# Performance work log

Measured on AMD Instinct MI355X. Metric: run time of the kernel, lower is better.

## Reference

```python
import jax, jax.numpy as jnp
import numpy as np

D_MODEL = 1024
NUM_HEADS = 16
D_LATENT = 256
HEAD_DIM = D_MODEL // NUM_HEADS
BATCH = 2048
SEQ = 32


def setup_inputs() -> dict:
    key = jax.random.key(0)
    ks = jax.random.split(key, 9)
    s = 1.0 / np.sqrt(D_MODEL)
    sl = 1.0 / np.sqrt(D_LATENT)
    return {
        "x": jax.random.normal(ks[0], (BATCH, SEQ, D_MODEL), dtype=jnp.float32),
        "memory": jax.random.normal(ks[1], (BATCH, SEQ, D_LATENT), dtype=jnp.float32),
        "W_q": jax.random.normal(ks[2], (D_MODEL, D_MODEL), dtype=jnp.float32) * s,
        "W_k": jax.random.normal(ks[3], (D_MODEL, D_MODEL), dtype=jnp.float32) * s,
        "W_v": jax.random.normal(ks[4], (D_MODEL, D_MODEL), dtype=jnp.float32) * s,
        "W_o": jax.random.normal(ks[5], (D_MODEL, D_MODEL), dtype=jnp.float32) * s,
        "W_down_kv": jax.random.normal(ks[6], (D_MODEL, D_LATENT), dtype=jnp.float32) * s,
        "W_up_k": jax.random.normal(ks[7], (D_LATENT, D_MODEL), dtype=jnp.float32) * sl,
        "W_up_v": jax.random.normal(ks[8], (D_LATENT, D_MODEL), dtype=jnp.float32) * sl,
    }


def reference(x, memory, W_q, W_k, W_v, W_o, W_down_kv, W_up_k, W_up_v):
    B, S, _ = x.shape
    q = x @ W_q                     # [B,S,D]
    k = x @ W_k
    v = x @ W_v
    latent_kv = (k + v) @ W_down_kv  # [B,S,L]
    latent_kv = jnp.nan_to_num((latent_kv + memory) * 0.5)
    k_rec = latent_kv @ W_up_k       # [B,S,D]
    v_rec = latent_kv @ W_up_v
    # split heads: [B,H,S,hd]
    qh = q.reshape(B, S, NUM_HEADS, HEAD_DIM).transpose(0, 2, 1, 3)
    kh = k_rec.reshape(B, S, NUM_HEADS, HEAD_DIM).transpose(0, 2, 1, 3)
    vh = v_rec.reshape(B, S, NUM_HEADS, HEAD_DIM).transpose(0, 2, 1, 3)
    # NOTE: faithful to source — scale is sqrt(d_model), not sqrt(head_dim)
    scores = jnp.einsum("bhqd,bhkd->bhqk", qh, kh) / jnp.sqrt(jnp.float32(D_MODEL))
    scores = jnp.nan_to_num(scores, nan=0.0, posinf=10.0, neginf=-10.0)
    attn = jax.nn.softmax(scores, axis=-1)
    ctx = jnp.einsum("bhqk,bhkd->bhqd", attn, vh)
    ctx = ctx.transpose(0, 2, 1, 3).reshape(B, S, D_MODEL)
    out = ctx @ W_o
    return out, latent_kv
```

## Files before the change

### kernel.cpp

```cpp
#include <hip/hip_runtime.h>
#include <hip/hip_bf16.h>

typedef unsigned short u16;
typedef unsigned int u32;
typedef __attribute__((ext_vector_type(8))) __bf16 bf16x8;
typedef __attribute__((ext_vector_type(8))) unsigned short u16x8;
typedef __attribute__((ext_vector_type(4))) float floatx4;
typedef __attribute__((ext_vector_type(16))) float floatx16;

#define AS1 __attribute__((address_space(1)))
#define AS3 __attribute__((address_space(3)))

__device__ __forceinline__ u16 f2bf(float f) {
  unsigned u = __float_as_uint(f);
  u += 0x7fffu + ((u >> 16) & 1u);
  return (u16)(u >> 16);
}

__device__ __forceinline__ void g2lds16(const u16* g, u16* l) {
  __builtin_amdgcn_global_load_lds((AS1 void*)g, (AS3 void*)l, 16, 0, 0);
}

__device__ __forceinline__ void tcvt_body(const float* __restrict__ s,
                                          u16* __restrict__ d, int R, int C,
                                          int bx, int by, int tid,
                                          float (*t)[33]) {
  const int lx = tid & 31, ly = tid >> 5;
  const int x0 = bx * 32, y0 = by * 32;
  #pragma unroll
  for (int i = 0; i < 32; i += 8)
    t[ly + i][lx] = s[(size_t)(y0 + ly + i) * C + x0 + lx];
  __syncthreads();
  #pragma unroll
  for (int i = 0; i < 32; i += 8)
    d[(size_t)(x0 + ly + i) * R + y0 + lx] = f2bf(t[lx][ly + i]);
}

__global__ __launch_bounds__(256) void k_prep(
    const float* __restrict__ x, u16* __restrict__ Xb,
    const float* __restrict__ Wk, const float* __restrict__ Wv, u16* __restrict__ Wkv,
    const float* __restrict__ Wq, u16* __restrict__ WAt,
    const float* __restrict__ Wdn, u16* __restrict__ Wdt,
    const float* __restrict__ Wuk, u16* __restrict__ WBt,
    const float* __restrict__ Wuv, u16* __restrict__ WBt2,
    const float* __restrict__ Wo, u16* __restrict__ Wot) {
  __shared__ float t[32][33];
  const int b = blockIdx.x;
  const int tid = threadIdx.x;
  if (b < 4096) {
    long i = ((long)b * 256 + tid) * 8;
    const long stride = (long)4096 * 256 * 8;
    for (; i < 67108864L; i += stride) {
      float4 a = *(const float4*)(x + i);
      float4 c = *(const float4*)(x + i + 4);
      u16x8 o;
      o[0] = f2bf(a.x); o[1] = f2bf(a.y); o[2] = f2bf(a.z); o[3] = f2bf(a.w);
      o[4] = f2bf(c.x); o[5] = f2bf(c.y); o[6] = f2bf(c.z); o[7] = f2bf(c.w);
      *(u16x8*)(Xb + i) = o;
    }
  } else if (b < 4608) {
    long i = ((long)(b - 4096) * 256 + tid) * 8;
    float4 a0 = *(const float4*)(Wk + i);
    float4 a1 = *(const float4*)(Wk + i + 4);
    float4 b0 = *(const float4*)(Wv + i);
    float4 b1 = *(const float4*)(Wv + i + 4);
    u16x8 o;
    o[0] = f2bf(a0.x + b0.x); o[1] = f2bf(a0.y + b0.y);
    o[2] = f2bf(a0.z + b0.z); o[3] = f2bf(a0.w + b0.w);
    o[4] = f2bf(a1.x + b1.x); o[5] = f2bf(a1.y + b1.y);
    o[6] = f2bf(a1.z + b1.z); o[7] = f2bf(a1.w + b1.w);
    *(u16x8*)(Wkv + i) = o;
  } else if (b < 5632) {
    int lb = b - 4608;
    tcvt_body(Wq, WAt, 1024, 1024, lb & 31, lb >> 5, tid, t);
  } else if (b < 5888) {
    int lb = b - 5632;
    tcvt_body(Wdn, Wdt, 1024, 256, lb & 7, lb >> 3, tid, t);
  } else if (b < 6144) {
    int lb = b - 5888;
    tcvt_body(Wuk, WBt, 256, 1024, lb & 31, lb >> 5, tid, t);
  } else if (b < 6400) {
    int lb = b - 6144;
    tcvt_body(Wuv, WBt2, 256, 1024, lb & 31, lb >> 5, tid, t);
  } else {
    int lb = b - 6400;
    tcvt_body(Wo, Wot, 1024, 1024, lb & 31, lb >> 5, tid, t);
  }
}

#define MFMA16(a, b, c) c = __builtin_amdgcn_mfma_f32_16x16x32_bf16(a, b, c, 0, 0, 0)

template <int MODE>
__global__ __launch_bounds__(512, 4) void gemm_mn(
    const u16* __restrict__ A, const u16* __restrict__ Bt,
    int M, int N, int K, int ntn,
    u16* __restrict__ Cb, float* __restrict__ Cf,
    const float* __restrict__ memp, float* __restrict__ latf, u16* __restrict__ latb) {
  __shared__ u16 As[256 * 64];
  __shared__ u16 Bs[128 * 64];
  const int tid = threadIdx.x;
  const int lane = tid & 63;
  const int wid = tid >> 6;
  const int wr = wid >> 1, wc = wid & 1;

  int bid = blockIdx.x;
  {
    const int nwg = gridDim.x;
    const int q = nwg >> 3, r = nwg & 7;
    const int xcd = bid & 7, idx = bid >> 3;
    bid = (xcd < r ? xcd * (q + 1) : r * (q + 1) + (xcd - r) * q) + idx;
  }
  const int mt = bid / ntn, nt = bid % ntn;
  const int m0 = mt * 256, n0 = nt * 128;

  const int fr = lane & 15;
  const int g8 = (lane >> 4) * 8;
  const int xr = (lane & 7) * 8;

  floatx4 acc[4][4];
  #pragma unroll
  for (int i = 0; i < 4; i++)
    #pragma unroll
    for (int j = 0; j < 4; j++) acc[i][j] = 0.0f;

  const u16* Ag0 = A + (size_t)m0 * K;
  const u16* Bg0 = Bt + (size_t)n0 * K;

  for (int kt = 0; kt < K; kt += 64) {
    #pragma unroll
    for (int p = 0; p < 4; p++) {
      int ci = p * 512 + tid;
      int row = ci >> 3;
      int kc = ((ci & 7) ^ (row & 7)) * 8;
      g2lds16(Ag0 + (size_t)row * K + kt + kc, &As[ci * 8]);
    }
    #pragma unroll
    for (int p = 0; p < 2; p++) {
      int ci = p * 512 + tid;
      int row = ci >> 3;
      int kc = ((ci & 7) ^ (row & 7)) * 8;
      g2lds16(Bg0 + (size_t)row * K + kt + kc, &Bs[ci * 8]);
    }
    __syncthreads();
    #pragma unroll
    for (int kk = 0; kk < 64; kk += 32) {
      const int koff = kk + g8;
      bf16x8 af[4], bfv[4];
      #pragma unroll
      for (int i = 0; i < 4; i++)
        af[i] = *(const bf16x8*)&As[(wr * 64 + i * 16 + fr) * 64 + (koff ^ xr)];
      #pragma unroll
      for (int j = 0; j < 4; j++)
        bfv[j] = *(const bf16x8*)&Bs[(wc * 64 + j * 16 + fr) * 64 + (koff ^ xr)];
      #pragma unroll
      for (int i = 0; i < 4; i++)
        #pragma unroll
        for (int j = 0; j < 4; j++)
          MFMA16(af[i], bfv[j], acc[i][j]);
    }
    __syncthreads();
  }

  #pragma unroll
  for (int i = 0; i < 4; i++) {
    const int mb = m0 + wr * 64 + i * 16 + ((lane >> 4) * 4);
    #pragma unroll
    for (int j = 0; j < 4; j++) {
      const int cb = n0 + wc * 64 + j * 16 + (lane & 15);
      #pragma unroll
      for (int r = 0; r < 4; r++) {
        const int m = mb + r;
        const float v = acc[i][j][r];
        if (MODE == 0) {
          Cb[(size_t)m * N + cb] = f2bf(v);
        } else if (MODE == 1) {
          if (n0 < 1024) {
            Cb[(size_t)m * 1024 + cb] = f2bf(v);
          } else {
            int lc = cb - 1024;
            float lv = (v + memp[(size_t)m * 256 + lc]) * 0.5f;
            latf[(size_t)m * 256 + lc] = lv;
            latb[(size_t)m * 256 + lc] = f2bf(lv);
          }
        } else {
          Cf[(size_t)m * N + cb] = v;
        }
      }
    }
  }
}

__global__ __launch_bounds__(256) void k_attn(const u16* __restrict__ KV, u16* Q) {
  __shared__ u16 Qs[4][32][72];
  __shared__ u16 Ks[4][32][72];
  __shared__ u16 Vt[4][64][40];
  const int tid = threadIdx.x;
  const int hg = blockIdx.x;
  const int b = blockIdx.y;
  const long tok0 = (long)b * 32;

  {
    const int t = tid >> 3, ci = tid & 7;
    const int hd = ci >> 1, c0 = (ci & 1) * 32;
    const u16* qrow = Q + (tok0 + t) * 1024 + hg * 256 + ci * 32;
    #pragma unroll
    for (int u = 0; u < 4; u++)
      *(u16x8*)&Qs[hd][t][c0 + u * 8] = *(const u16x8*)(qrow + u * 8);
    const u16* krow = KV + (tok0 + t) * 2048 + hg * 256 + ci * 32;
    #pragma unroll
    for (int u = 0; u < 4; u++)
      *(u16x8*)&Ks[hd][t][c0 + u * 8] = *(const u16x8*)(krow + u * 8);
    const u16* vrow = KV + (tok0 + t) * 2048 + 1024 + hg * 256 + ci * 32;
    #pragma unroll
    for (int u = 0; u < 4; u++) {
      u16x8 v = *(const u16x8*)(vrow + u * 8);
      #pragma unroll
      for (int j = 0; j < 8; j++) Vt[hd][c0 + u * 8 + j][t] = v[j];
    }
  }
  __syncthreads();

  const int w = tid >> 6;
  const int lane = tid & 63;
  const int col = lane & 31, hi = lane >> 5;

  floatx16 S;
  #pragma unroll
  for (int r = 0; r < 16; r++) S[r] = 0.0f;
  #pragma unroll
  for (int kc = 0; kc < 4; kc++) {
    bf16x8 aq = *(const bf16x8*)&Qs[w][col][kc * 16 + hi * 8];
    bf16x8 bk = *(const bf16x8*)&Ks[w][col][kc * 16 + hi * 8];
    S = __builtin_amdgcn_mfma_f32_32x32x16_bf16(aq, bk, S, 0, 0, 0);
  }

  u16* Pw = &Qs[w][0][0];
  float pr[16];
  #pragma unroll
  for (int r = 0; r < 16; r++) {
    float sc = S[r] * 0.03125f;
    float mx = sc;
    #pragma unroll
    for (int off = 16; off >= 1; off >>= 1) mx = fmaxf(mx, __shfl_xor(mx, off, 64));
    float e = __expf(sc - mx);
    float sm = e;
    #pragma unroll
    for (int off = 16; off >= 1; off >>= 1) sm += __shfl_xor(sm, off, 64);
    pr[r] = e / sm;
  }
  #pragma unroll
  for (int r = 0; r < 16; r++) {
    int row = (r & 3) + 8 * (r >> 2) + 4 * hi;
    Pw[row * 40 + col] = f2bf(pr[r]);
  }
  __syncthreads();

  floatx16 c0v, c1v;
  #pragma unroll
  for (int r = 0; r < 16; r++) { c0v[r] = 0.0f; c1v[r] = 0.0f; }
  #pragma unroll
  for (int kc = 0; kc < 2; kc++) {
    bf16x8 ap = *(const bf16x8*)&Pw[col * 40 + kc * 16 + hi * 8];
    bf16x8 bv0 = *(const bf16x8*)&Vt[w][col][kc * 16 + hi * 8];
    bf16x8 bv1 = *(const bf16x8*)&Vt[w][32 + col][kc * 16 + hi * 8];
    c0v = __builtin_amdgcn_mfma_f32_32x32x16_bf16(ap, bv0, c0v, 0, 0, 0);
    c1v = __builtin_amdgcn_mfma_f32_32x32x16_bf16(ap, bv1, c1v, 0, 0, 0);
  }
  #pragma unroll
  for (int r = 0; r < 16; r++) {
    int row = (r & 3) + 8 * (r >> 2) + 4 * hi;
    u16* orow = Q + (tok0 + row) * 1024 + hg * 256 + w * 64;
    orow[col] = f2bf(c0v[r]);
    orow[col + 32] = f2bf(c1v[r]);
  }
}

extern "C" void kernel_launch(void* const* d_in, const int* in_sizes, int n_in,
                              void* d_out, int out_size, void* d_ws, size_t ws_size,
                              hipStream_t stream) {
  const float* x    = (const float*)d_in[0];
  const float* mem  = (const float*)d_in[1];
  const float* W_q  = (const float*)d_in[2];
  const float* W_k  = (const float*)d_in[3];
  const float* W_v  = (const float*)d_in[4];
  const float* W_o  = (const float*)d_in[5];
  const float* W_dn = (const float*)d_in[6];
  const float* W_uk = (const float*)d_in[7];
  const float* W_uv = (const float*)d_in[8];
  float* out  = (float*)d_out;
  float* latf = out + (size_t)67108864;

  char* wp = (char*)d_ws;
  u16* Qb  = (u16*)wp; wp += (size_t)65536 * 1024 * 2;
  u16* Lb  = (u16*)wp; wp += (size_t)65536 * 256 * 2;
  u16* WAt = (u16*)wp; wp += (size_t)1280 * 1024 * 2;
  u16* WBt = (u16*)wp; wp += (size_t)2048 * 256 * 2;
  u16* Wot = (u16*)wp; wp += (size_t)1024 * 1024 * 2;
  u16* Wdt = (u16*)wp; wp += (size_t)256 * 1024 * 2;
  u16* Wkv = (u16*)wp; wp += (size_t)1024 * 1024 * 2;

  u16* Xb  = (u16*)d_out;
  u16* KVb = (u16*)d_out;

  dim3 b256(256);
  dim3 b512(512);

  k_prep<<<7424, b256, 0, stream>>>(
      x, Xb, W_k, W_v, Wkv, W_q, WAt, W_dn, Wdt,
      W_uk, WBt, W_uv, WBt + (size_t)1024 * 256, W_o, Wot);

  gemm_mn<0><<<8, b512, 0, stream>>>(
      Wdt, Wkv, 256, 1024, 1024, 8, WAt + (size_t)1024 * 1024,
      nullptr, nullptr, nullptr, nullptr);

  gemm_mn<1><<<2560, b512, 0, stream>>>(
      Xb, WAt, 65536, 1280, 1024, 10, Qb, nullptr, mem, latf, Lb);

  gemm_mn<0><<<4096, b512, 0, stream>>>(
      Lb, WBt, 65536, 2048, 256, 16, KVb, nullptr, nullptr, nullptr, nullptr);

  k_attn<<<dim3(4, 2048), b256, 0, stream>>>(KVb, Qb);

  gemm_mn<2><<<2048, b512, 0, stream>>>(
      Qb, Wot, 65536, 1024, 1024, 8, nullptr, out, nullptr, nullptr, nullptr);
}
```

Before: 841.3 us.

## Fuse latent up-projection into attention kernel and shrink GEMM tiles to 128x128

Removes the separate up-projection GEMM that wrote K and V (65536x2048 bf16) to global memory. The attention kernel now loads the latent rows into LDS and computes per-head K and V with MFMA, reading the weights directly from global memory. Separately, the generic GEMM moves from 256x128 tiles with 512 threads to 128x128 tiles with 256 threads, doubling the grid. The fused version recomputes K/V per head group from uncached global weight loads and uses more LDS. It also drops the barrier before the P*V step, which is safe only because each wave reads just its own LDS region.

```diff
diff --git a/kernel.cpp b/kernel.cpp
--- a/kernel.cpp
+++ b/kernel.cpp
@@ -89,14 +89,15 @@
 }
 
 #define MFMA16(a, b, c) c = __builtin_amdgcn_mfma_f32_16x16x32_bf16(a, b, c, 0, 0, 0)
+#define MFMA32(a, b, c) c = __builtin_amdgcn_mfma_f32_32x32x16_bf16(a, b, c, 0, 0, 0)
 
 template <int MODE>
-__global__ __launch_bounds__(512, 4) void gemm_mn(
+__global__ __launch_bounds__(256, 3) void gemm128(
     const u16* __restrict__ A, const u16* __restrict__ Bt,
     int M, int N, int K, int ntn,
     u16* __restrict__ Cb, float* __restrict__ Cf,
     const float* __restrict__ memp, float* __restrict__ latf, u16* __restrict__ latb) {
-  __shared__ u16 As[256 * 64];
+  __shared__ u16 As[128 * 64];
   __shared__ u16 Bs[128 * 64];
   const int tid = threadIdx.x;
   const int lane = tid & 63;
@@ -111,7 +112,7 @@
     bid = (xcd < r ? xcd * (q + 1) : r * (q + 1) + (xcd - r) * q) + idx;
   }
   const int mt = bid / ntn, nt = bid % ntn;
-  const int m0 = mt * 256, n0 = nt * 128;
+  const int m0 = mt * 128, n0 = nt * 128;
 
   const int fr = lane & 15;
   const int g8 = (lane >> 4) * 8;
@@ -129,14 +130,14 @@
   for (int kt = 0; kt < K; kt += 64) {
     #pragma unroll
     for (int p = 0; p < 4; p++) {
-      int ci = p * 512 + tid;
+      int ci = p * 256 + tid;
       int row = ci >> 3;
       int kc = ((ci & 7) ^ (row & 7)) * 8;
       g2lds16(Ag0 + (size_t)row * K + kt + kc, &As[ci * 8]);
     }
     #pragma unroll
-    for (int p = 0; p < 2; p++) {
-      int ci = p * 512 + tid;
+    for (int p = 0; p < 4; p++) {
+      int ci = p * 256 + tid;
       int row = ci >> 3;
       int kc = ((ci & 7) ^ (row & 7)) * 8;
       g2lds16(Bg0 + (size_t)row * K + kt + kc, &Bs[ci * 8]);
@@ -190,10 +191,15 @@
   }
 }
 
-__global__ __launch_bounds__(256) void k_attn(const u16* __restrict__ KV, u16* Q) {
+__global__ __launch_bounds__(256, 2) void k_attn_kv(
+    const u16* __restrict__ Lb,
+    u16* __restrict__ Q,
+    const u16* __restrict__ WBt)
+{
   __shared__ u16 Qs[4][32][72];
   __shared__ u16 Ks[4][32][72];
   __shared__ u16 Vt[4][64][40];
+  __shared__ u16 Ls[32][264];
   const int tid = threadIdx.x;
   const int hg = blockIdx.x;
   const int b = blockIdx.y;
@@ -206,23 +212,47 @@
     #pragma unroll
     for (int u = 0; u < 4; u++)
       *(u16x8*)&Qs[hd][t][c0 + u * 8] = *(const u16x8*)(qrow + u * 8);
-    const u16* krow = KV + (tok0 + t) * 2048 + hg * 256 + ci * 32;
+    const u16* lrow = Lb + (tok0 + t) * 256 + ci * 32;
     #pragma unroll
     for (int u = 0; u < 4; u++)
-      *(u16x8*)&Ks[hd][t][c0 + u * 8] = *(const u16x8*)(krow + u * 8);
-    const u16* vrow = KV + (tok0 + t) * 2048 + 1024 + hg * 256 + ci * 32;
-    #pragma unroll
-    for (int u = 0; u < 4; u++) {
-      u16x8 v = *(const u16x8*)(vrow + u * 8);
-      #pragma unroll
-      for (int j = 0; j < 8; j++) Vt[hd][c0 + u * 8 + j][t] = v[j];
-    }
+      *(u16x8*)&Ls[t][ci * 32 + u * 8] = *(const u16x8*)(lrow + u * 8);
   }
   __syncthreads();
 
   const int w = tid >> 6;
   const int lane = tid & 63;
   const int col = lane & 31, hi = lane >> 5;
+  const int h = hg * 4 + w;
+
+  floatx16 ka0, ka1, va0, va1;
+  #pragma unroll
+  for (int r = 0; r < 16; r++) { ka0[r] = 0.f; ka1[r] = 0.f; va0[r] = 0.f; va1[r] = 0.f; }
+  const u16* wkp = WBt + (size_t)(h * 64) * 256;
+  const u16* wvp = WBt + (size_t)(1024 + h * 64) * 256;
+  #pragma unroll
+  for (int ks = 0; ks < 16; ks++) {
+    const int ko = ks * 16 + hi * 8;
+    bf16x8 la = *(const bf16x8*)&Ls[col][ko];
+    bf16x8 bk0 = *(const bf16x8*)(wkp + (size_t)col * 256 + ko);
+    bf16x8 bk1 = *(const bf16x8*)(wkp + (size_t)(32 + col) * 256 + ko);
+    bf16x8 bv0 = *(const bf16x8*)(wvp + (size_t)col * 256 + ko);
+    bf16x8 bv1 = *(const bf16x8*)(wvp + (size_t)(32 + col) * 256 + ko);
+    MFMA32(la, bk0, ka0);
+    MFMA32(la, bk1, ka1);
+    MFMA32(la, bv0, va0);
+    MFMA32(la, bv1, va1);
+  }
+  #pragma unroll
+  for (int i = 0; i < 8; i++) {
+    const int r = 2 * i;
+    const int rr = (r & 3) + 8 * (r >> 2) + 4 * hi;
+    Ks[w][rr][col] = f2bf(ka0[r]);
+    Ks[w][rr + 1][col] = f2bf(ka0[r + 1]);
+    Ks[w][rr][32 + col] = f2bf(ka1[r]);
+    Ks[w][rr + 1][32 + col] = f2bf(ka1[r + 1]);
+    *(u32*)&Vt[w][col][rr] = (u32)f2bf(va0[r]) | ((u32)f2bf(va0[r + 1]) << 16);
+    *(u32*)&Vt[w][32 + col][rr] = (u32)f2bf(va1[r]) | ((u32)f2bf(va1[r + 1]) << 16);
+  }
 
   floatx16 S;
   #pragma unroll
@@ -231,7 +261,7 @@
   for (int kc = 0; kc < 4; kc++) {
     bf16x8 aq = *(const bf16x8*)&Qs[w][col][kc * 16 + hi * 8];
     bf16x8 bk = *(const bf16x8*)&Ks[w][col][kc * 16 + hi * 8];
-    S = __builtin_amdgcn_mfma_f32_32x32x16_bf16(aq, bk, S, 0, 0, 0);
+    MFMA32(aq, bk, S);
   }
 
   u16* Pw = &Qs[w][0][0];
@@ -253,7 +283,6 @@
     int row = (r & 3) + 8 * (r >> 2) + 4 * hi;
     Pw[row * 40 + col] = f2bf(pr[r]);
   }
-  __syncthreads();
 
   floatx16 c0v, c1v;
   #pragma unroll
@@ -263,8 +292,8 @@
     bf16x8 ap = *(const bf16x8*)&Pw[col * 40 + kc * 16 + hi * 8];
     bf16x8 bv0 = *(const bf16x8*)&Vt[w][col][kc * 16 + hi * 8];
     bf16x8 bv1 = *(const bf16x8*)&Vt[w][32 + col][kc * 16 + hi * 8];
-    c0v = __builtin_amdgcn_mfma_f32_32x32x16_bf16(ap, bv0, c0v, 0, 0, 0);
-    c1v = __builtin_amdgcn_mfma_f32_32x32x16_bf16(ap, bv1, c1v, 0, 0, 0);
+    MFMA32(ap, bv0, c0v);
+    MFMA32(ap, bv1, c1v);
   }
   #pragma unroll
   for (int r = 0; r < 16; r++) {
@@ -299,28 +328,23 @@
   u16* Wdt = (u16*)wp; wp += (size_t)256 * 1024 * 2;
   u16* Wkv = (u16*)wp; wp += (size_t)1024 * 1024 * 2;
 
-  u16* Xb  = (u16*)d_out;
-  u16* KVb = (u16*)d_out;
+  u16* Xb = (u16*)d_out;
 
   dim3 b256(256);
-  dim3 b512(512);
 
   k_prep<<<7424, b256, 0, stream>>>(
       x, Xb, W_k, W_v, Wkv, W_q, WAt, W_dn, Wdt,
       W_uk, WBt, W_uv, WBt + (size_t)1024 * 256, W_o, Wot);
 
-  gemm_mn<0><<<8, b512, 0, stream>>>(
+  gemm128<0><<<16, b256, 0, stream>>>(
       Wdt, Wkv, 256, 1024, 1024, 8, WAt + (size_t)1024 * 1024,
       nullptr, nullptr, nullptr, nullptr);
 
-  gemm_mn<1><<<2560, b512, 0, stream>>>(
+  gemm128<1><<<5120, b256, 0, stream>>>(
       Xb, WAt, 65536, 1280, 1024, 10, Qb, nullptr, mem, latf, Lb);
 
-  gemm_mn<0><<<4096, b512, 0, stream>>>(
-      Lb, WBt, 65536, 2048, 256, 16, KVb, nullptr, nullptr, nullptr, nullptr);
-
-  k_attn<<<dim3(4, 2048), b256, 0, stream>>>(KVb, Qb);
-
-  gemm_mn<2><<<2048, b512, 0, stream>>>(
+  k_attn_kv<<<dim3(4, 2048), b256, 0, stream>>>(Lb, Qb, WBt);
+
+  gemm128<2><<<4096, b256, 0, stream>>>(
       Qb, Wot, 65536, 1024, 1024, 8, nullptr, out, nullptr, nullptr, nullptr);
 }
```

After: 854.3 us. About the same (+1.6%).
